# Kernel optimization log

Measured on AMD Instinct MI355X. Metric: run time of the kernel, lower is better.

The kernel has to match this reference:

```python
import jax, jax.numpy as jnp
import numpy as np
from jax import lax

B, T_Y, T_X = 16, 1600, 400
MEL_C, TXT_C, MAS_C = 80, 512, 384
HID = MAS_C * 2          # SwiGLUConvFFN hidden width (mas_channels*2)
NEG = -1e9


def setup_inputs() -> dict:
    key = jax.random.key(0)
    ks = jax.random.split(key, 20)
    p = lambda k, s: jax.random.normal(k, s, jnp.float32) * 0.02
    return {
        "mel_hidden_states": jax.random.normal(ks[0], (B, T_Y, MEL_C), jnp.float32),
        "text_hidden_states": jax.random.normal(ks[1], (B, T_X, TXT_C), jnp.float32),
        # mel SwiGLU conv-FFN (kernel 5): in->2*HID, gate, HID->MAS_C
        "mel_w1": p(ks[2], (2 * HID, MEL_C, 5)), "mel_b1": jnp.zeros((2 * HID,), jnp.float32),
        "mel_w2": p(ks[3], (MAS_C, HID, 5)),     "mel_b2": jnp.zeros((MAS_C,), jnp.float32),
        # text SwiGLU conv-FFN (kernel 3)
        "txt_w1": p(ks[4], (2 * HID, TXT_C, 3)), "txt_b1": jnp.zeros((2 * HID,), jnp.float32),
        "txt_w2": p(ks[5], (MAS_C, HID, 3)),     "txt_b2": jnp.zeros((MAS_C,), jnp.float32),
        # SimpleAttention query/key projections (value proj does not affect returned outputs)
        "wq": p(ks[6], (MAS_C, MAS_C)), "bq": jnp.zeros((MAS_C,), jnp.float32),
        "wk": p(ks[7], (MAS_C, MAS_C)), "bk": jnp.zeros((MAS_C,), jnp.float32),
        "x_lens": jax.random.randint(ks[8], (B,), T_X // 2, T_X + 1).astype(jnp.int32),
        "y_lens": jax.random.randint(ks[9], (B,), T_Y // 2, T_Y + 1).astype(jnp.int32),
    }


def _conv_ffn(x, pad_mask, w1, b1, w2, b2):
    """SwiGLU/ReGLU conv FFN. x:(B,T,C), pad_mask:(B,T) True=padded."""
    keep = (~pad_mask)[:, None, :].astype(x.dtype)          # (B,1,T)
    h = jnp.transpose(x, (0, 2, 1)) * keep                  # (B,C,T)
    dn = ("NCH", "OIH", "NCH")
    h = lax.conv_general_dilated(h, w1, (1,), "SAME", dimension_numbers=dn) + b1[None, :, None]
    a, g = jnp.split(h, 2, axis=1)
    h = a * jax.nn.relu(g) * keep                           # relugt gating
    h = lax.conv_general_dilated(h, w2, (1,), "SAME", dimension_numbers=dn) + b2[None, :, None]
    return jnp.transpose(h * keep, (0, 2, 1))               # (B,T,out)


def _mas_single(logp, t_x, t_y):
    """Glow-TTS maximum_path for one item. logp:(T_X,T_Y). Returns hard path (T_X,T_Y)."""
    xi = jnp.arange(T_X)
    yi = jnp.arange(T_Y)
    valid = (xi[:, None] < t_x) & (yi[None, :] < t_y) & (xi[:, None] <= yi[None, :])
    lp = jnp.where(valid, logp, NEG)

    def fstep(prev, col):                                   # prev:(T_X,), col:(T_X,)
        shifted = jnp.concatenate([jnp.full((1,), NEG, prev.dtype), prev[:-1]])
        cur = col + jnp.maximum(prev, shifted)
        return cur, cur

    init = jnp.where(xi == 0, 0.0, NEG).astype(logp.dtype)
    _, v = lax.scan(fstep, init, lp.T)                      # v:(T_Y,T_X) DP table

    def bstep(x, y):                                        # backtrack from y=T_Y-1 down
        active = y < t_y
        row = (xi == x) & active
        vp = v[y - 1]
        dec = (x > 0) & ((x == y) | (vp[jnp.maximum(x - 1, 0)] > vp[x]))
        new_x = jnp.where(active & (y > 0) & dec, x - 1, x)
        return new_x, row

    _, rows = lax.scan(bstep, t_x - 1, jnp.arange(T_Y - 1, -1, -1))
    return rows[::-1].T.astype(jnp.float32)                 # (T_X,T_Y)


def _safe_log(t, eps=1e-6):
    return jnp.nan_to_num(jnp.log(t + eps), nan=eps)


def reference(mel_hidden_states, text_hidden_states,
              mel_w1, mel_b1, mel_w2, mel_b2,
              txt_w1, txt_b1, txt_w2, txt_b2,
              wq, bq, wk, bk, x_lens, y_lens):
    x_mask = jnp.arange(T_X)[None, :] >= x_lens[:, None]    # (B,T_X) True=padded
    y_mask = jnp.arange(T_Y)[None, :] >= y_lens[:, None]    # (B,T_Y)

    text_proj = _conv_ffn(text_hidden_states, x_mask, txt_w1, txt_b1, txt_w2, txt_b2)
    mel_proj = _conv_ffn(mel_hidden_states, y_mask, mel_w1, mel_b1, mel_w2, mel_b2)

    q = mel_proj @ wq.T + bq                                # (B,T_Y,D)
    k = text_proj @ wk.T + bk                               # (B,T_X,D)
    scores = jnp.einsum("byd,bxd->byx", q, k) / (MAS_C ** 0.5)
    # expand_masks: mask==0 only where query AND key are both padded (faithful to source)
    both_pad = y_mask[:, :, None] & x_mask[:, None, :]
    scores = jnp.where(both_pad, jnp.float32(-1e-9), scores)
    attn_w = jax.nn.softmax(scores, axis=-1)                # (B,T_Y,T_X)

    avg_attn = attn_w[:, None]                              # (B,1,T_Y,T_X)
    attn_logprob = _safe_log(avg_attn)

    mas_in = jnp.transpose(attn_logprob[:, 0], (0, 2, 1))   # (B,T_X,T_Y)
    attn_hard = lax.stop_gradient(jax.vmap(_mas_single)(mas_in, x_lens, y_lens))
    attn_hard_dur = attn_hard.sum(2)                        # (B,T_X)
    return avg_attn, attn_logprob, attn_hard, attn_hard_dur
```

## Files before the change

### kernel.cpp

```cpp
#include <hip/hip_runtime.h>
#include <cstdint>

#define B 16
#define TY 1600
#define TX 400
#define MAS 384
#define HID 768
#define NEGV -1e9f

typedef __bf16 bf16x8 __attribute__((ext_vector_type(8)));
typedef float  f32x4  __attribute__((ext_vector_type(4)));
typedef float  f32x16 __attribute__((ext_vector_type(16)));

__device__ __forceinline__ f32x4 mfma16(bf16x8 a, bf16x8 b, f32x4 c) {
  return __builtin_amdgcn_mfma_f32_16x16x32_bf16(a, b, c, 0, 0, 0);
}
__device__ __forceinline__ f32x16 mfma32(bf16x8 a, bf16x8 b, f32x16 c) {
  return __builtin_amdgcn_mfma_f32_32x32x16_bf16(a, b, c, 0, 0, 0);
}

__global__ void split_pad_k(const float* __restrict__ in, __bf16* __restrict__ oh,
                            __bf16* __restrict__ ol, int CIN, int CINP, long n) {
  long i = (long)blockIdx.x * 256 + threadIdx.x;
  if (i >= n) return;
  long row = i / CINP; int ci = (int)(i - row * CINP);
  float v = (ci < CIN) ? in[row * CIN + ci] : 0.f;
  __bf16 h = (__bf16)v;
  oh[i] = h; ol[i] = (__bf16)(v - (float)h);
}

__global__ void wsplit_k(const float* __restrict__ w, __bf16* __restrict__ oh,
                         __bf16* __restrict__ ol, int CIN, int K_, int CINP, long n) {
  long i = (long)blockIdx.x * 256 + threadIdx.x;
  if (i >= n) return;
  long kdspan = (long)K_ * CINP;
  long nn = i / kdspan; int kd = (int)(i - nn * kdspan);
  int k = kd / CINP, ci = kd - k * CINP;
  float v = (ci < CIN) ? w[(nn * CIN + ci) * K_ + k] : 0.f;
  __bf16 h = (__bf16)v;
  oh[i] = h; ol[i] = (__bf16)(v - (float)h);
}

__global__ void tsplit_k(const float* __restrict__ in, __bf16* __restrict__ oh,
                         __bf16* __restrict__ ol, int JTOT, long n) {
  long i = (long)blockIdx.x * 256 + threadIdx.x;
  if (i >= n) return;
  int m = (int)(i / JTOT), j = (int)(i - (long)m * JTOT);
  float v = in[i];
  long o = (long)j * 384 + m;
  __bf16 h = (__bf16)v;
  oh[o] = h; ol[o] = (__bf16)(v - (float)h);
}

__global__ void fold_bias_k(const float* __restrict__ wq, const float* __restrict__ b,
                            float* __restrict__ o) {
  int n = threadIdx.x;
  float s = 0.f;
  for (int m = 0; m < 384; ++m) s = fmaf(wq[n * 384 + m], b[m], s);
  o[n] = s;
}

template<int KK>
__global__ __launch_bounds__(256)
void fold_mfma(const __bf16* __restrict__ xh, const __bf16* __restrict__ xl,
               const __bf16* __restrict__ wh, const __bf16* __restrict__ wl,
               __bf16* __restrict__ oh, __bf16* __restrict__ ol)
{
  constexpr int CINP = 384, ROWS = 64, STRIDE = 65;
  __shared__ float4 xs[8 * STRIDE];
  const int t0 = blockIdx.x * 64, n0 = blockIdx.y * 128;
  const int tid = threadIdx.x, wn = tid >> 6, lane = tid & 63;
  const int lr = lane & 15, lg = lane >> 4;
  const f32x4 Z4 = {0.f, 0.f, 0.f, 0.f};
  f32x4 acc[4][2];
  #pragma unroll
  for (int m = 0; m < 4; ++m) { acc[m][0] = Z4; acc[m][1] = Z4; }

  #pragma unroll 1
  for (int ci0 = 0; ci0 < CINP; ci0 += 32) {
    __syncthreads();
    for (int e = tid; e < ROWS * 8; e += 256) {
      int row = e >> 3, sc = e & 7, spl = sc >> 2, cg = sc & 3;
      int t = t0 + row;
      xs[(spl * 4 + cg) * STRIDE + row] =
          *(const float4*)((spl ? xl : xh) + (size_t)t * CINP + ci0 + cg * 8);
    }
    __syncthreads();
    bf16x8 ah[4], al[4];
    #pragma unroll
    for (int mf = 0; mf < 4; ++mf) {
      int row = mf * 16 + lr;
      ah[mf] = *(const bf16x8*)&xs[lg * STRIDE + row];
      al[mf] = *(const bf16x8*)&xs[(4 + lg) * STRIDE + row];
    }
    size_t kd = (size_t)ci0 + lg * 8;
    bf16x8 bh[2], bl[2];
    #pragma unroll
    for (int nf = 0; nf < 2; ++nf) {
      int nc = n0 + wn * 32 + nf * 16 + lr;
      bh[nf] = *(const bf16x8*)(wh + (size_t)nc * 384 + kd);
      bl[nf] = *(const bf16x8*)(wl + (size_t)nc * 384 + kd);
    }
    #pragma unroll
    for (int nf = 0; nf < 2; ++nf)
      #pragma unroll
      for (int mf = 0; mf < 4; ++mf) acc[mf][nf] = mfma16(ah[mf], bh[nf], acc[mf][nf]);
    #pragma unroll
    for (int nf = 0; nf < 2; ++nf)
      #pragma unroll
      for (int mf = 0; mf < 4; ++mf) acc[mf][nf] = mfma16(ah[mf], bl[nf], acc[mf][nf]);
    #pragma unroll
    for (int nf = 0; nf < 2; ++nf)
      #pragma unroll
      for (int mf = 0; mf < 4; ++mf) acc[mf][nf] = mfma16(al[mf], bh[nf], acc[mf][nf]);
  }
  #pragma unroll
  for (int nf = 0; nf < 2; ++nf) {
    int c = n0 + wn * 32 + nf * 16 + lr;
    #pragma unroll
    for (int mf = 0; mf < 4; ++mf) {
      #pragma unroll
      for (int r = 0; r < 4; ++r) {
        int j = t0 + mf * 16 + lg * 4 + r;
        int k = j % KK, ci = j / KK;
        size_t o = (size_t)((((ci >> 4) * KK + k) * 2 + ((ci >> 3) & 1)) * 3072)
                 + (size_t)c * 8 + (ci & 7);
        float v = acc[mf][nf][r];
        __bf16 vh = (__bf16)v;
        oh[o] = vh; ol[o] = (__bf16)(v - (float)vh);
      }
    }
  }
}

template<int CINP, int K, int T>
__global__ __launch_bounds__(256)
void conv1_mfma(const __bf16* __restrict__ xh, const __bf16* __restrict__ xl,
                const __bf16* __restrict__ wh, const __bf16* __restrict__ wl,
                const float* __restrict__ bias, const int* __restrict__ lens,
                __bf16* __restrict__ hh, __bf16* __restrict__ hl)
{
  constexpr int BM = 128, PAD = K / 2, ROWS = BM + K - 1, KD = K * CINP;
  __shared__ float4 xs[8 * ROWS];
  const int b = blockIdx.z, t0 = blockIdx.x * BM, n0 = blockIdx.y * 64;
  const int tid = threadIdx.x, wid = tid >> 6, lane = tid & 63;
  const int wm = wid >> 1, wn = wid & 1, lr = lane & 15, lg = lane >> 4;
  const int len = lens[b];
  const f32x4 Z4 = {0.f, 0.f, 0.f, 0.f};
  f32x4 acc_a[4][2], acc_g[4][2];
  #pragma unroll
  for (int m = 0; m < 4; ++m)
    #pragma unroll
    for (int n = 0; n < 2; ++n) { acc_a[m][n] = Z4; acc_g[m][n] = Z4; }

  #pragma unroll 1
  for (int ci0 = 0; ci0 < CINP; ci0 += 32) {
    __syncthreads();
    for (int e = tid; e < ROWS * 8; e += 256) {
      int row = e >> 3, sc = e & 7, spl = sc >> 2, cg = sc & 3;
      int t = t0 + row - PAD;
      float4 v = {0.f, 0.f, 0.f, 0.f};
      if (t >= 0 && t < len)
        v = *(const float4*)((spl ? xl : xh) + ((size_t)b * T + t) * CINP + ci0 + cg * 8);
      xs[(spl * 4 + cg) * ROWS + row] = v;
    }
    __syncthreads();
    #pragma unroll
    for (int k = 0; k < K; ++k) {
      bf16x8 ah[4], al[4];
      #pragma unroll
      for (int mf = 0; mf < 4; ++mf) {
        int row = wm * 64 + mf * 16 + lr + k;
        ah[mf] = *(const bf16x8*)&xs[lg * ROWS + row];
        al[mf] = *(const bf16x8*)&xs[(4 + lg) * ROWS + row];
      }
      size_t kd = (size_t)k * CINP + ci0 + lg * 8;
      #pragma unroll
      for (int nf = 0; nf < 2; ++nf) {
        int na = n0 + wn * 32 + nf * 16 + lr;
        bf16x8 bah = *(const bf16x8*)(wh + (size_t)na * KD + kd);
        bf16x8 bal = *(const bf16x8*)(wl + (size_t)na * KD + kd);
        bf16x8 bgh = *(const bf16x8*)(wh + (size_t)(na + HID) * KD + kd);
        bf16x8 bgl = *(const bf16x8*)(wl + (size_t)(na + HID) * KD + kd);
        #pragma unroll
        for (int mf = 0; mf < 4; ++mf) {
          acc_a[mf][nf] = mfma16(ah[mf], bah, acc_a[mf][nf]);
          acc_a[mf][nf] = mfma16(ah[mf], bal, acc_a[mf][nf]);
          acc_a[mf][nf] = mfma16(al[mf], bah, acc_a[mf][nf]);
          acc_g[mf][nf] = mfma16(ah[mf], bgh, acc_g[mf][nf]);
          acc_g[mf][nf] = mfma16(ah[mf], bgl, acc_g[mf][nf]);
          acc_g[mf][nf] = mfma16(al[mf], bgh, acc_g[mf][nf]);
        }
      }
    }
  }
  #pragma unroll
  for (int nf = 0; nf < 2; ++nf) {
    int c = n0 + wn * 32 + nf * 16 + lr;
    float ba = bias[c], bg = bias[c + HID];
    #pragma unroll
    for (int mf = 0; mf < 4; ++mf) {
      #pragma unroll
      for (int r = 0; r < 4; ++r) {
        int t = t0 + wm * 64 + mf * 16 + lg * 4 + r;
        if (t < T) {
          float a = acc_a[mf][nf][r] + ba;
          float g = acc_g[mf][nf][r] + bg;
          float v = a * fmaxf(g, 0.f);
          __bf16 vh = (__bf16)v;
          size_t o = ((size_t)b * T + t) * HID + c;
          hh[o] = vh;
          hl[o] = (__bf16)(v - (float)vh);
        }
      }
    }
  }
}

template<int K, int T, bool STORET>
__global__ __launch_bounds__(256)
void conv2_mfma(const __bf16* __restrict__ xh, const __bf16* __restrict__ xl,
                const __bf16* __restrict__ wh, const __bf16* __restrict__ wl,
                const float* __restrict__ bias, const float* __restrict__ ab,
                const int* __restrict__ lens, float* __restrict__ out)
{
  constexpr int CINP = 768, BM = 128, PAD = K / 2, ROWS = BM + K - 1, STRIDE = ROWS + 1;
  constexpr int BROWS = K * 2;
  __shared__ float4 xa[4 * STRIDE];
  __shared__ float4 bs[2 * BROWS * 192];
  const int b = blockIdx.z, t0 = blockIdx.x * BM, n0 = blockIdx.y * 192;
  const int tid = threadIdx.x, wid = tid >> 6, lane = tid & 63;
  const int wm = wid >> 1, wn = wid & 1, lc = lane & 31, lk = lane >> 5;
  const int len = lens[b];
  f32x16 acc[2][3];
  #pragma unroll
  for (int m = 0; m < 2; ++m)
    #pragma unroll
    for (int n = 0; n < 3; ++n)
      #pragma unroll
      for (int r = 0; r < 16; ++r) acc[m][n][r] = 0.f;

  #pragma unroll 1
  for (int s = 0; s < 48; ++s) {
    __syncthreads();
    for (int e = tid; e < ROWS * 4; e += 256) {
      int row = e >> 2, sc = e & 3, spl = sc >> 1, cg = sc & 1;
      int t = t0 + row - PAD;
      float4 v = {0.f, 0.f, 0.f, 0.f};
      if (t >= 0 && t < len)
        v = *(const float4*)((spl ? xl : xh) + ((size_t)b * T + t) * CINP + s * 16 + cg * 8);
      xa[(spl * 2 + cg) * STRIDE + row] = v;
    }
    for (int r = wid; r < 2 * BROWS; r += 4) {
      int spl = r / BROWS, rr = r - spl * BROWS;
      const char* src = (const char*)((spl ? wl : wh) + (size_t)(s * BROWS + rr) * 3072
                                      + (size_t)n0 * 8) + (size_t)lane * 16;
      char* dst = (char*)&bs[r * 192];
      #pragma unroll
      for (int i = 0; i < 3; ++i)
        __builtin_amdgcn_global_load_lds(
            (const __attribute__((address_space(1))) void*)(src + i * 1024),
            (__attribute__((address_space(3))) void*)(dst + i * 1024), 16, 0, 0);
    }
    __syncthreads();
    #pragma unroll
    for (int k = 0; k < K; ++k) {
      bf16x8 ah[2], al[2], bh[3], bl[3];
      #pragma unroll
      for (int mf = 0; mf < 2; ++mf) {
        int row = wm * 64 + mf * 32 + lc + k;
        ah[mf] = *(const bf16x8*)&xa[lk * STRIDE + row];
        al[mf] = *(const bf16x8*)&xa[(2 + lk) * STRIDE + row];
      }
      #pragma unroll
      for (int nf = 0; nf < 3; ++nf) {
        int col = wn * 96 + nf * 32 + lc;
        bh[nf] = *(const bf16x8*)&bs[(k * 2 + lk) * 192 + col];
        bl[nf] = *(const bf16x8*)&bs[(BROWS + k * 2 + lk) * 192 + col];
      }
      #pragma unroll
      for (int nf = 0; nf < 3; ++nf)
        #pragma unroll
        for (int mf = 0; mf < 2; ++mf)
          acc[mf][nf] = mfma32(ah[mf], bh[nf], acc[mf][nf]);
      #pragma unroll
      for (int nf = 0; nf < 3; ++nf)
        #pragma unroll
        for (int mf = 0; mf < 2; ++mf)
          acc[mf][nf] = mfma32(ah[mf], bl[nf], acc[mf][nf]);
      #pragma unroll
      for (int nf = 0; nf < 3; ++nf)
        #pragma unroll
        for (int mf = 0; mf < 2; ++mf)
          acc[mf][nf] = mfma32(al[mf], bh[nf], acc[mf][nf]);
    }
  }
  #pragma unroll
  for (int nf = 0; nf < 3; ++nf) {
    int c = n0 + wn * 96 + nf * 32 + lc;
    float bb = bias[c], aB = ab[c];
    #pragma unroll
    for (int mf = 0; mf < 2; ++mf) {
      #pragma unroll
      for (int r = 0; r < 16; ++r) {
        int t = t0 + wm * 64 + mf * 32 + (r & 3) + 8 * (r >> 2) + 4 * lk;
        if (t < T) {
          float v = acc[mf][nf][r] + bb;
          if (t >= len) v = 0.f;
          v += aB;
          if (STORET) out[((size_t)b * MAS + c) * T + t] = v;
          else        out[((size_t)b * T + t) * MAS + c] = v;
        }
      }
    }
  }
}

__global__ __launch_bounds__(512)
void scores_k(const float* __restrict__ q, const float* __restrict__ kT,
              const int* __restrict__ xl, const int* __restrict__ yl,
              float* __restrict__ oattn, float* __restrict__ ologp)
{
  __shared__ float qs[16 * 384];
  __shared__ float tmp[8];
  const int b = blockIdx.y, y0 = blockIdx.x * 16, tid = threadIdx.x;
  for (int e = tid; e < 16 * 384; e += 512)
    qs[e] = q[((size_t)b * TY + (y0 + e / 384)) * 384 + (e - (e / 384) * 384)];
  __syncthreads();
  float acc[16];
  #pragma unroll
  for (int i = 0; i < 16; ++i) acc[i] = 0.f;
  const int x = tid;
  if (x < TX) {
    const float* kb = kT + (size_t)b * MAS * TX + x;
    for (int d = 0; d < 384; d += 4) {
      float k0 = kb[(size_t)(d + 0) * TX], k1 = kb[(size_t)(d + 1) * TX];
      float k2 = kb[(size_t)(d + 2) * TX], k3 = kb[(size_t)(d + 3) * TX];
      #pragma unroll
      for (int yy = 0; yy < 16; ++yy) {
        float4 qv = *(const float4*)&qs[yy * 384 + d];
        acc[yy] = fmaf(qv.x, k0, fmaf(qv.y, k1, fmaf(qv.z, k2, fmaf(qv.w, k3, acc[yy]))));
      }
    }
  }
  const int xlen = xl[b], ylen = yl[b];
  const float scale = 0.05103103630798288f;
  const bool xpad = (x >= xlen);
  const int wv = tid >> 6, ln = tid & 63;
  #pragma unroll 1
  for (int yy = 0; yy < 16; ++yy) {
    int y = y0 + yy;
    float s = -3.0e38f;
    if (x < TX) {
      s = acc[yy] * scale;
      if (xpad && (y >= ylen)) s = -1e-9f;
    }
    float m = s;
    for (int off = 32; off; off >>= 1) m = fmaxf(m, __shfl_xor(m, off));
    if (ln == 0) tmp[wv] = m;
    __syncthreads();
    float mx = fmaxf(fmaxf(fmaxf(tmp[0], tmp[1]), fmaxf(tmp[2], tmp[3])),
                     fmaxf(fmaxf(tmp[4], tmp[5]), fmaxf(tmp[6], tmp[7])));
    __syncthreads();
    float e = (x < TX) ? expf(s - mx) : 0.f;
    float sm = e;
    for (int off = 32; off; off >>= 1) sm += __shfl_xor(sm, off);
    if (ln == 0) tmp[wv] = sm;
    __syncthreads();
    float tot = tmp[0] + tmp[1] + tmp[2] + tmp[3] + tmp[4] + tmp[5] + tmp[6] + tmp[7];
    __syncthreads();
    if (x < TX) {
      float w = e / tot;
      size_t o = ((size_t)b * TY + y) * TX + x;
      oattn[o] = w;
      ologp[o] = logf(w + 1e-6f);
    }
  }
}

#define MAS_LD(blkv, buf) do {                                           \
    int base_ = (blkv) * 4;                                              \
    _Pragma("unroll")                                                    \
    for (int d_ = 0; d_ < 4; ++d_) {                                     \
      int yr_ = base_ + d_; if (yr_ > TY - 1) yr_ = TY - 1;              \
      const float* r_ = lpb + (size_t)yr_ * TX;                          \
      buf[d_ * 3 + 0] = *(const float4*)(r_ + lb0);                      \
      buf[d_ * 3 + 1] = *(const float4*)(r_ + lb1);                      \
      buf[d_ * 3 + 2] = *(const float4*)(r_ + lb2);                      \
    } } while (0)

#define MAS_BLK(blkv, buf, PAR) do {                                     \
    float h0 = __shfl_up(w[8], 1),  h1 = __shfl_up(w[9], 1);             \
    float h2 = __shfl_up(w[10], 1), h3 = __shfl_up(w[11], 1);            \
    w[0] = lane ? h0 : NEGV; w[1] = lane ? h1 : NEGV;                    \
    w[2] = lane ? h2 : NEGV; w[3] = lane ? h3 : NEGV;                    \
    const int y0_ = (blkv) * 4;                                          \
    const bool ph1_ = (y0_ < TX);                                        \
    _Pragma("unroll")                                                    \
    for (int d_ = 0; d_ < 4; ++d_) {                                     \
      const int y_ = y0_ + d_;                                           \
      float lp[12];                                                      \
      _Pragma("unroll")                                                  \
      for (int k_ = 0; k_ < 3; ++k_) {                                   \
        float4 v_ = buf[d_ * 3 + k_];                                    \
        lp[k_*4+0] = v_.x + wxm[k_*4+0]; lp[k_*4+1] = v_.y + wxm[k_*4+1];\
        lp[k_*4+2] = v_.z + wxm[k_*4+2]; lp[k_*4+3] = v_.w + wxm[k_*4+3];\
      }                                                                  \
      if (ph1_) {                                                        \
        int c_ = y_ - p0;                                                \
        _Pragma("unroll")                                                \
        for (int i_ = 0; i_ < 12; ++i_) lp[i_] = (i_ <= c_) ? lp[i_] : NEGV; \
      }                                                                  \
      unsigned byte_ = 0;                                                \
      _Pragma("unroll")                                                  \
      for (int j_ = 0; j_ < 8; ++j_)                                     \
        byte_ |= (w[j_ + 3] > w[j_ + 4]) ? (1u << j_) : 0u;              \
      bitsacc |= (unsigned long long)byte_ << (((PAR) * 4 + d_) * 8);    \
      float nw[12];                                                      \
      nw[0] = lp[0] + w[0];                                              \
      _Pragma("unroll")                                                  \
      for (int i_ = 1; i_ < 12; ++i_) nw[i_] = lp[i_] + fmaxf(w[i_], w[i_ - 1]); \
      _Pragma("unroll")                                                  \
      for (int i_ = 0; i_ < 12; ++i_) w[i_] = nw[i_];                    \
    } } while (0)

#define MAS_ST(oddblk) do {                                              \
    *(unsigned long long*)(bb8 + ((size_t)((oddblk) >> 1)) * 512 + (size_t)lane * 8) = bitsacc; \
    bitsacc = 0ULL; } while (0)

__global__ __launch_bounds__(64, 1)
void mas_k(const float* __restrict__ logprob, const int* __restrict__ xl,
           const int* __restrict__ yl, unsigned char* __restrict__ bits,
           float* __restrict__ hard, float* __restrict__ dur)
{
  const int b = blockIdx.x;
  const int lane = threadIdx.x;
  const int xlen = xl[b], ylen = yl[b];
  const float* lpb = logprob + (size_t)b * TY * TX;
  unsigned char* bb8 = bits + (size_t)b * 102400;
  const int p0 = lane * 8 - 4;
  int t;
  t = p0;     if (t < 0) t = 0; if (t > 396) t = 396; const int lb0 = t;
  t = p0 + 4; if (t < 0) t = 0; if (t > 396) t = 396; const int lb1 = t;
  t = p0 + 8; if (t < 0) t = 0; if (t > 396) t = 396; const int lb2 = t;

  float w[12], wxm[12];
  #pragma unroll
  for (int i = 0; i < 12; ++i) {
    int p = p0 + i;
    wxm[i] = (p >= 0 && p < xlen) ? 0.f : NEGV;
    w[i] = (p == 0) ? 0.f : NEGV;
  }

  float4 buf0[12], buf1[12], buf2[12], buf3[12];
  MAS_LD(0, buf0); MAS_LD(1, buf1); MAS_LD(2, buf2); MAS_LD(3, buf3);
  unsigned long long bitsacc = 0ULL;
  const int nblk = (ylen + 3) >> 2;
  int blk = 0;
  #pragma unroll 1
  for (; blk + 3 < nblk; blk += 4) {
    __builtin_amdgcn_sched_barrier(0);
    MAS_BLK(blk, buf0, 0);     MAS_LD(blk + 4, buf0);
    __builtin_amdgcn_sched_barrier(0);
    MAS_BLK(blk + 1, buf1, 1); MAS_LD(blk + 5, buf1); MAS_ST(blk + 1);
    __builtin_amdgcn_sched_barrier(0);
    MAS_BLK(blk + 2, buf2, 0); MAS_LD(blk + 6, buf2);
    __builtin_amdgcn_sched_barrier(0);
    MAS_BLK(blk + 3, buf3, 1); MAS_LD(blk + 7, buf3); MAS_ST(blk + 3);
  }
  {
    const int r = nblk - blk;
    if (r > 0) MAS_BLK(blk, buf0, 0);
    if (r > 1) { MAS_BLK(blk + 1, buf1, 1); MAS_ST(blk + 1); }
    if (r > 2) MAS_BLK(blk + 2, buf2, 0);
    if (r == 1 || r == 3) {
      *(unsigned long long*)(bb8 + ((size_t)((blk + r - 1) >> 1)) * 512 + (size_t)lane * 8) = bitsacc;
    }
  }

  __threadfence();
  __syncthreads();

  int x = xlen - 1;
  int cnt = 0;
  float* hb = hard + (size_t)b * TX * TY;
  float* db = dur + (size_t)b * TX;

  #pragma unroll 1
  for (int ycur = ylen - 1; ycur >= 0; ycur -= 64) {
    int lo = x - 63; if (lo < 0) lo = 0;
    const int wb = (lo >> 3) & ~3;
    int ry = ycur - lane;
    unsigned w0 = 0, w1 = 0, w2 = 0;
    if (ry >= 0) {
      const unsigned char* p = bb8 + (size_t)(ry >> 3) * 512 + (ry & 7);
      unsigned bt_[12];
      #pragma unroll
      for (int j = 0; j < 12; ++j) bt_[j] = p[(size_t)(wb + j) * 8];
      w0 = bt_[0] | (bt_[1] << 8) | (bt_[2] << 16) | (bt_[3] << 24);
      w1 = bt_[4] | (bt_[5] << 8) | (bt_[6] << 16) | (bt_[7] << 24);
      w2 = bt_[8] | (bt_[9] << 8) | (bt_[10] << 16) | (bt_[11] << 24);
    }
    const int rows = (ycur + 1 < 64) ? (ycur + 1) : 64;
    #pragma unroll 1
    for (int s = 0; s < rows; s += 8) {
      const int cnt8 = (rows - s < 8) ? (rows - s) : 8;
      unsigned r0[8], r1[8], r2[8];
      #pragma unroll
      for (int u = 0; u < 8; ++u) {
        r0[u] = (unsigned)__builtin_amdgcn_readlane((int)w0, s + u);
        r1[u] = (unsigned)__builtin_amdgcn_readlane((int)w1, s + u);
        r2[u] = (unsigned)__builtin_amdgcn_readlane((int)w2, s + u);
      }
      #pragma unroll
      for (int u = 0; u < 8; ++u) {
        if (u < cnt8) {
          const int yy = ycur - s - u;
          ++cnt;
          if (yy > 0 && x > 0) {
            const int boff = (x >> 3) - wb;
            const unsigned word = (boff < 4) ? r0[u] : ((boff < 8) ? r1[u] : r2[u]);
            const unsigned byte = word >> ((boff & 3) * 8);
            if ((x == yy) || ((byte >> (x & 7)) & 1)) {
              for (int q = lane; q < cnt; q += 64) hb[(size_t)x * TY + yy + q] = 1.0f;
              if (lane == 0) db[x] = (float)cnt;
              cnt = 0;
              --x;
            }
          }
        }
      }
    }
  }
  for (int q = lane; q < cnt; q += 64) hb[(size_t)x * TY + q] = 1.0f;
  if (lane == 0) db[x] = (float)cnt;
}

extern "C" void kernel_launch(void* const* d_in, const int* in_sizes, int n_in,
                              void* d_out, int out_size, void* d_ws, size_t ws_size,
                              hipStream_t stream) {
  const float* mel_x  = (const float*)d_in[0];
  const float* txt_x  = (const float*)d_in[1];
  const float* mel_w1 = (const float*)d_in[2];
  const float* mel_b1 = (const float*)d_in[3];
  const float* mel_w2 = (const float*)d_in[4];
  const float* mel_b2 = (const float*)d_in[5];
  const float* txt_w1 = (const float*)d_in[6];
  const float* txt_b1 = (const float*)d_in[7];
  const float* txt_w2 = (const float*)d_in[8];
  const float* txt_b2 = (const float*)d_in[9];
  const float* wq     = (const float*)d_in[10];
  const float* bq     = (const float*)d_in[11];
  const float* wk     = (const float*)d_in[12];
  const float* bk     = (const float*)d_in[13];
  const int*   xl     = (const int*)d_in[14];
  const int*   yl     = (const int*)d_in[15];

  char* wsb = (char*)d_ws;
  constexpr size_t MXH   = 0;
  constexpr size_t MXL   = MXH   + 4915200;
  constexpr size_t TXH   = MXL   + 4915200;
  constexpr size_t TXL   = TXH   + 6553600;
  constexpr size_t KTF   = TXH;
  constexpr size_t WFMH  = TXL   + 6553600;
  constexpr size_t WFML  = WFMH  + 2949120;
  constexpr size_t WFTH  = WFML  + 2949120;
  constexpr size_t WFTL  = WFTH  + 1769472;
  constexpr size_t B2M   = WFTL  + 1769472;
  constexpr size_t B2T   = B2M   + 2048;
  constexpr size_t HH    = B2T   + 2048;
  constexpr size_t HL    = HH    + 39321600;
  constexpr size_t BITS  = MXH;
  constexpr size_t SCR   = HL    + 39321600;
  constexpr size_t W1MH  = SCR;
  constexpr size_t W1ML  = W1MH  + 1474560;
  constexpr size_t W1TH  = W1ML  + 1474560;
  constexpr size_t W1TL  = W1TH  + 4718592;
  constexpr size_t WQH   = W1TL  + 4718592;
  constexpr size_t WQL   = WQH   + 294912;
  constexpr size_t WKH   = WQL   + 294912;
  constexpr size_t WKL   = WKH   + 294912;
  constexpr size_t W2TMH = WKL   + 294912;
  constexpr size_t W2TML = W2TMH + 2949120;
  constexpr size_t W2TTH = W2TML + 2949120;
  constexpr size_t W2TTL = W2TTH + 1769472;
  constexpr size_t QF    = SCR;

  float* out = (float*)d_out;
  float* o_attn = out;
  float* o_logp = out + (size_t)10240000;
  float* o_hard = out + (size_t)20480000;
  float* o_dur  = out + (size_t)30720000;

  hipMemsetAsync(o_hard, 0, (size_t)(10240000 + 6400) * sizeof(float), stream);

  split_pad_k<<<9600, 256, 0, stream>>>(mel_x, (__bf16*)(wsb + MXH), (__bf16*)(wsb + MXL), 80, 96, 2457600L);
  split_pad_k<<<12800, 256, 0, stream>>>(txt_x, (__bf16*)(wsb + TXH), (__bf16*)(wsb + TXL), 512, 512, 3276800L);
  wsplit_k<<<2880, 256, 0, stream>>>(mel_w1, (__bf16*)(wsb + W1MH), (__bf16*)(wsb + W1ML), 80, 5, 96, 737280L);
  wsplit_k<<<9216, 256, 0, stream>>>(txt_w1, (__bf16*)(wsb + W1TH), (__bf16*)(wsb + W1TL), 512, 3, 512, 2359296L);
  wsplit_k<<<576, 256, 0, stream>>>(wq, (__bf16*)(wsb + WQH), (__bf16*)(wsb + WQL), 384, 1, 384, 147456L);
  wsplit_k<<<576, 256, 0, stream>>>(wk, (__bf16*)(wsb + WKH), (__bf16*)(wsb + WKL), 384, 1, 384, 147456L);
  tsplit_k<<<5760, 256, 0, stream>>>(mel_w2, (__bf16*)(wsb + W2TMH), (__bf16*)(wsb + W2TML), 3840, 1474560L);
  tsplit_k<<<3456, 256, 0, stream>>>(txt_w2, (__bf16*)(wsb + W2TTH), (__bf16*)(wsb + W2TTL), 2304, 884736L);
  fold_mfma<5><<<dim3(60, 3), 256, 0, stream>>>(
      (const __bf16*)(wsb + W2TMH), (const __bf16*)(wsb + W2TML),
      (const __bf16*)(wsb + WQH), (const __bf16*)(wsb + WQL),
      (__bf16*)(wsb + WFMH), (__bf16*)(wsb + WFML));
  fold_mfma<3><<<dim3(36, 3), 256, 0, stream>>>(
      (const __bf16*)(wsb + W2TTH), (const __bf16*)(wsb + W2TTL),
      (const __bf16*)(wsb + WKH), (const __bf16*)(wsb + WKL),
      (__bf16*)(wsb + WFTH), (__bf16*)(wsb + WFTL));
  fold_bias_k<<<1, 384, 0, stream>>>(wq, mel_b2, (float*)(wsb + B2M));
  fold_bias_k<<<1, 384, 0, stream>>>(wk, txt_b2, (float*)(wsb + B2T));

  conv1_mfma<512, 3, 400><<<dim3(4, 12, B), 256, 0, stream>>>(
      (const __bf16*)(wsb + TXH), (const __bf16*)(wsb + TXL),
      (const __bf16*)(wsb + W1TH), (const __bf16*)(wsb + W1TL),
      txt_b1, xl, (__bf16*)(wsb + HH), (__bf16*)(wsb + HL));
  conv2_mfma<3, 400, true><<<dim3(4, 2, B), 256, 0, stream>>>(
      (const __bf16*)(wsb + HH), (const __bf16*)(wsb + HL),
      (const __bf16*)(wsb + WFTH), (const __bf16*)(wsb + WFTL),
      (const float*)(wsb + B2T), bk, xl, (float*)(wsb + KTF));

  conv1_mfma<96, 5, 1600><<<dim3(13, 12, B), 256, 0, stream>>>(
      (const __bf16*)(wsb + MXH), (const __bf16*)(wsb + MXL),
      (const __bf16*)(wsb + W1MH), (const __bf16*)(wsb + W1ML),
      mel_b1, yl, (__bf16*)(wsb + HH), (__bf16*)(wsb + HL));
  conv2_mfma<5, 1600, false><<<dim3(13, 2, B), 256, 0, stream>>>(
      (const __bf16*)(wsb + HH), (const __bf16*)(wsb + HL),
      (const __bf16*)(wsb + WFMH), (const __bf16*)(wsb + WFML),
      (const float*)(wsb + B2M), bq, yl, (float*)(wsb + QF));

  scores_k<<<dim3(100, B), 512, 0, stream>>>(
      (const float*)(wsb + QF), (const float*)(wsb + KTF), xl, yl, o_attn, o_logp);
  mas_k<<<B, 64, 0, stream>>>(o_logp, xl, yl, (unsigned char*)(wsb + BITS), o_hard, o_dur);
}
```

Before: 1.555 ms.

## Stage MAS logprob rows via async global-to-LDS loads and keep backpointers in LDS

The serial MAS dynamic-programming kernel now streams logprob rows in 16-row groups into a double-buffered LDS ring using global_load_lds, gated by an explicit vmcnt wait. Previously it used register-prefetched float4 loads. The backpointer bitmask also moves from a global workspace buffer into a 100KB LDS array, which removes the global stores, the thread fence and the global reads during backtracking. The goal is to cut memory latency on the latency-bound single-wave-per-batch path. The cost is about 150KB of LDS per block, and correctness now depends on hand-counted waitcnt values.

```diff
diff --git a/kernel.cpp b/kernel.cpp
--- a/kernel.cpp
+++ b/kernel.cpp
@@ -378,66 +378,16 @@
   }
 }
 
-#define MAS_LD(blkv, buf) do {                                           \
-    int base_ = (blkv) * 4;                                              \
-    _Pragma("unroll")                                                    \
-    for (int d_ = 0; d_ < 4; ++d_) {                                     \
-      int yr_ = base_ + d_; if (yr_ > TY - 1) yr_ = TY - 1;              \
-      const float* r_ = lpb + (size_t)yr_ * TX;                          \
-      buf[d_ * 3 + 0] = *(const float4*)(r_ + lb0);                      \
-      buf[d_ * 3 + 1] = *(const float4*)(r_ + lb1);                      \
-      buf[d_ * 3 + 2] = *(const float4*)(r_ + lb2);                      \
-    } } while (0)
-
-#define MAS_BLK(blkv, buf, PAR) do {                                     \
-    float h0 = __shfl_up(w[8], 1),  h1 = __shfl_up(w[9], 1);             \
-    float h2 = __shfl_up(w[10], 1), h3 = __shfl_up(w[11], 1);            \
-    w[0] = lane ? h0 : NEGV; w[1] = lane ? h1 : NEGV;                    \
-    w[2] = lane ? h2 : NEGV; w[3] = lane ? h3 : NEGV;                    \
-    const int y0_ = (blkv) * 4;                                          \
-    const bool ph1_ = (y0_ < TX);                                        \
-    _Pragma("unroll")                                                    \
-    for (int d_ = 0; d_ < 4; ++d_) {                                     \
-      const int y_ = y0_ + d_;                                           \
-      float lp[12];                                                      \
-      _Pragma("unroll")                                                  \
-      for (int k_ = 0; k_ < 3; ++k_) {                                   \
-        float4 v_ = buf[d_ * 3 + k_];                                    \
-        lp[k_*4+0] = v_.x + wxm[k_*4+0]; lp[k_*4+1] = v_.y + wxm[k_*4+1];\
-        lp[k_*4+2] = v_.z + wxm[k_*4+2]; lp[k_*4+3] = v_.w + wxm[k_*4+3];\
-      }                                                                  \
-      if (ph1_) {                                                        \
-        int c_ = y_ - p0;                                                \
-        _Pragma("unroll")                                                \
-        for (int i_ = 0; i_ < 12; ++i_) lp[i_] = (i_ <= c_) ? lp[i_] : NEGV; \
-      }                                                                  \
-      unsigned byte_ = 0;                                                \
-      _Pragma("unroll")                                                  \
-      for (int j_ = 0; j_ < 8; ++j_)                                     \
-        byte_ |= (w[j_ + 3] > w[j_ + 4]) ? (1u << j_) : 0u;              \
-      bitsacc |= (unsigned long long)byte_ << (((PAR) * 4 + d_) * 8);    \
-      float nw[12];                                                      \
-      nw[0] = lp[0] + w[0];                                              \
-      _Pragma("unroll")                                                  \
-      for (int i_ = 1; i_ < 12; ++i_) nw[i_] = lp[i_] + fmaxf(w[i_], w[i_ - 1]); \
-      _Pragma("unroll")                                                  \
-      for (int i_ = 0; i_ < 12; ++i_) w[i_] = nw[i_];                    \
-    } } while (0)
-
-#define MAS_ST(oddblk) do {                                              \
-    *(unsigned long long*)(bb8 + ((size_t)((oddblk) >> 1)) * 512 + (size_t)lane * 8) = bitsacc; \
-    bitsacc = 0ULL; } while (0)
-
 __global__ __launch_bounds__(64, 1)
 void mas_k(const float* __restrict__ logprob, const int* __restrict__ xl,
-           const int* __restrict__ yl, unsigned char* __restrict__ bits,
-           float* __restrict__ hard, float* __restrict__ dur)
+           const int* __restrict__ yl, float* __restrict__ hard, float* __restrict__ dur)
 {
+  __shared__ float ring[12800];
+  __shared__ unsigned char lbits[102400];
   const int b = blockIdx.x;
   const int lane = threadIdx.x;
   const int xlen = xl[b], ylen = yl[b];
   const float* lpb = logprob + (size_t)b * TY * TX;
-  unsigned char* bb8 = bits + (size_t)b * 102400;
   const int p0 = lane * 8 - 4;
   int t;
   t = p0;     if (t < 0) t = 0; if (t > 396) t = 396; const int lb0 = t;
@@ -452,33 +402,74 @@
     w[i] = (p == 0) ? 0.f : NEGV;
   }
 
-  float4 buf0[12], buf1[12], buf2[12], buf3[12];
-  MAS_LD(0, buf0); MAS_LD(1, buf1); MAS_LD(2, buf2); MAS_LD(3, buf3);
-  unsigned long long bitsacc = 0ULL;
-  const int nblk = (ylen + 3) >> 2;
-  int blk = 0;
+  const char* lpc = (const char*)lpb;
+  constexpr size_t maxgs = (size_t)TY * 1600 - 25600;
+  char* ringc = (char*)ring;
+  auto issue_group = [&](int g) {
+    size_t gs = (size_t)g * 25600; if (gs > maxgs) gs = maxgs;
+    const char* src = lpc + gs + (size_t)lane * 16;
+    char* dst = ringc + (g & 1) * 25600;
+    #pragma unroll
+    for (int i = 0; i < 25; ++i)
+      __builtin_amdgcn_global_load_lds(
+          (const __attribute__((address_space(1))) void*)(src + i * 1024),
+          (__attribute__((address_space(3))) void*)(dst + i * 1024), 16, 0, 0);
+  };
+
+  issue_group(0);
+  issue_group(1);
+
+  const int ngroups = (ylen + 15) >> 4;
   #pragma unroll 1
-  for (; blk + 3 < nblk; blk += 4) {
+  for (int g = 0; g < ngroups; ++g) {
+    asm volatile("s_waitcnt vmcnt(25)" ::: "memory");
     __builtin_amdgcn_sched_barrier(0);
-    MAS_BLK(blk, buf0, 0);     MAS_LD(blk + 4, buf0);
+    const float* half = ring + (g & 1) * 6400;
+    const int ybase = g * 16;
+    const bool phase1 = (ybase < TX);
+    unsigned long long bitsacc = 0ULL;
+    #pragma unroll
+    for (int d = 0; d < 4; ++d) {
+      float h0 = __shfl_up(w[8], 1),  h1 = __shfl_up(w[9], 1);
+      float h2 = __shfl_up(w[10], 1), h3 = __shfl_up(w[11], 1);
+      w[0] = lane ? h0 : NEGV; w[1] = lane ? h1 : NEGV;
+      w[2] = lane ? h2 : NEGV; w[3] = lane ? h3 : NEGV;
+      #pragma unroll
+      for (int r = 0; r < 4; ++r) {
+        const int row = d * 4 + r;
+        const int y = ybase + row;
+        const float4 v0 = *(const float4*)&half[row * 400 + lb0];
+        const float4 v1 = *(const float4*)&half[row * 400 + lb1];
+        const float4 v2 = *(const float4*)&half[row * 400 + lb2];
+        float lp[12] = {v0.x + wxm[0], v0.y + wxm[1], v0.z + wxm[2],  v0.w + wxm[3],
+                        v1.x + wxm[4], v1.y + wxm[5], v1.z + wxm[6],  v1.w + wxm[7],
+                        v2.x + wxm[8], v2.y + wxm[9], v2.z + wxm[10], v2.w + wxm[11]};
+        if (phase1) {
+          int c = y - p0;
+          #pragma unroll
+          for (int i = 0; i < 12; ++i) lp[i] = (i <= c) ? lp[i] : NEGV;
+        }
+        unsigned byte = 0;
+        #pragma unroll
+        for (int j = 0; j < 8; ++j)
+          byte |= (w[j + 3] > w[j + 4]) ? (1u << j) : 0u;
+        bitsacc |= (unsigned long long)byte << (((d & 1) * 4 + r) * 8);
+        float nw[12];
+        nw[0] = lp[0] + w[0];
+        #pragma unroll
+        for (int i = 1; i < 12; ++i) nw[i] = lp[i] + fmaxf(w[i], w[i - 1]);
+        #pragma unroll
+        for (int i = 0; i < 12; ++i) w[i] = nw[i];
+      }
+      if (d & 1) {
+        *(unsigned long long*)&lbits[(size_t)((ybase >> 3) + (d >> 1)) * 512 + (size_t)lane * 8] = bitsacc;
+        bitsacc = 0ULL;
+      }
+    }
     __builtin_amdgcn_sched_barrier(0);
-    MAS_BLK(blk + 1, buf1, 1); MAS_LD(blk + 5, buf1); MAS_ST(blk + 1);
-    __builtin_amdgcn_sched_barrier(0);
-    MAS_BLK(blk + 2, buf2, 0); MAS_LD(blk + 6, buf2);
-    __builtin_amdgcn_sched_barrier(0);
-    MAS_BLK(blk + 3, buf3, 1); MAS_LD(blk + 7, buf3); MAS_ST(blk + 3);
-  }
-  {
-    const int r = nblk - blk;
-    if (r > 0) MAS_BLK(blk, buf0, 0);
-    if (r > 1) { MAS_BLK(blk + 1, buf1, 1); MAS_ST(blk + 1); }
-    if (r > 2) MAS_BLK(blk + 2, buf2, 0);
-    if (r == 1 || r == 3) {
-      *(unsigned long long*)(bb8 + ((size_t)((blk + r - 1) >> 1)) * 512 + (size_t)lane * 8) = bitsacc;
-    }
-  }
-
-  __threadfence();
+    issue_group(g + 2);
+  }
+
   __syncthreads();
 
   int x = xlen - 1;
@@ -493,7 +484,7 @@
     int ry = ycur - lane;
     unsigned w0 = 0, w1 = 0, w2 = 0;
     if (ry >= 0) {
-      const unsigned char* p = bb8 + (size_t)(ry >> 3) * 512 + (ry & 7);
+      const unsigned char* p = lbits + (size_t)(ry >> 3) * 512 + (ry & 7);
       unsigned bt_[12];
       #pragma unroll
       for (int j = 0; j < 12; ++j) bt_[j] = p[(size_t)(wb + j) * 8];
@@ -570,7 +561,6 @@
   constexpr size_t B2T   = B2M   + 2048;
   constexpr size_t HH    = B2T   + 2048;
   constexpr size_t HL    = HH    + 39321600;
-  constexpr size_t BITS  = MXH;
   constexpr size_t SCR   = HL    + 39321600;
   constexpr size_t W1MH  = SCR;
   constexpr size_t W1ML  = W1MH  + 1474560;
@@ -633,5 +623,5 @@
 
   scores_k<<<dim3(100, B), 512, 0, stream>>>(
       (const float*)(wsb + QF), (const float*)(wsb + KTF), xl, yl, o_attn, o_logp);
-  mas_k<<<B, 64, 0, stream>>>(o_logp, xl, yl, (unsigned char*)(wsb + BITS), o_hard, o_dur);
-}
+  mas_k<<<B, 64, 0, stream>>>(o_logp, xl, yl, o_hard, o_dur);
+}
```

Measured after the change: 1.528 ms. No clear change (-1.7%).
